# Kernel tuning notes

Hardware: AMD Instinct MI355X
Metric: run time of the kernel (lower is better)

Reference implementation:

```python
import jax, jax.numpy as jnp
import numpy as np
from jax import lax

BN_EPS = 1e-5
SP_NEAR = 2


def fps(xyz, m):
    # xyz: [b, n, c] -> indices [b, m]; deterministic start at index 0
    b, n, _ = xyz.shape
    def step(carry, _):
        dist, far = carry
        centroid = jnp.take_along_axis(xyz, far[:, None, None], axis=1)  # [b,1,c]
        d = jnp.sum((xyz - centroid) ** 2, axis=-1)                      # [b,n]
        dist = jnp.minimum(dist, d)
        return (dist, jnp.argmax(dist, axis=-1).astype(jnp.int32)), far
    init = (jnp.full((b, n), jnp.inf, xyz.dtype), jnp.zeros((b,), jnp.int32))
    _, idxs = lax.scan(step, init, None, length=m)
    return jnp.transpose(idxs)  # [b, m]


def knn(x, k):
    # x: [b, n, c] -> k nearest (incl. self) indices [b, n, k]
    sq = jnp.sum(x * x, axis=-1)
    d = sq[:, :, None] + sq[:, None, :] - 2.0 * jnp.einsum('bnc,bmc->bnm', x, x)
    return lax.top_k(-d, k)[1]


def gather_cf(x, idx):
    # channel-first index_points: x [b, c, n], idx [b, ...] -> [b, c, *idx.shape[1:]]
    b, c = x.shape[:2]
    flat = idx.reshape(b, -1)
    g = jnp.take_along_axis(x, flat[:, None, :], axis=2)
    return g.reshape((b, c) + idx.shape[1:])


def gather_cl(x, idx):
    # channel-last index_points: x [b, n, c], idx [b, ...] -> [b, *idx.shape[1:], c]
    b, c = x.shape[0], x.shape[-1]
    flat = idx.reshape(b, -1)
    g = jnp.take_along_axis(x, flat[:, :, None], axis=1)
    return g.reshape((b,) + idx.shape[1:] + (c,))


def bn_act(x, gamma, beta, nd):
    # inference-mode BatchNorm (running mean 0, var 1) + exact GELU; Dropout is identity in eval
    shp = (1, -1) + (1,) * nd
    scale = 1.0 / jnp.sqrt(1.0 + BN_EPS)
    return jax.nn.gelu(gamma.reshape(shp) * (x * scale) + beta.reshape(shp), approximate=False)


def setup_inputs() -> dict:
    key = jax.random.key(0)
    ks = jax.random.split(key, 8)
    BS, SP_IN, SP_OUT, DN_IN, DN_OUT = 128, 256, 256, 128, 128
    N_STK, N_STK_PNT, COOR = 32, 32, 32
    return {
        'sparse_fea': jax.random.normal(ks[0], (BS, SP_IN, N_STK), jnp.float32),
        'dense_fea': jax.random.normal(ks[1], (BS, DN_IN, N_STK, N_STK_PNT), jnp.float32),
        'stk_coor': jax.random.normal(ks[2], (BS, N_STK, COOR), jnp.float32),
        'n_stk_center': 16,
        'sp_w': jax.random.normal(ks[3], (SP_OUT, 2 * SP_IN), jnp.float32) * 0.02,
        'sp_b': jnp.zeros((SP_OUT,), jnp.float32),
        'sp_g': jnp.ones((SP_OUT,), jnp.float32),
        'sp_beta': jnp.zeros((SP_OUT,), jnp.float32),
        'dn_w': jax.random.normal(ks[4], (DN_OUT, 2 * DN_IN), jnp.float32) * 0.02,
        'dn_b': jnp.zeros((DN_OUT,), jnp.float32),
        'dn_g': jnp.ones((DN_OUT,), jnp.float32),
        'dn_beta': jnp.zeros((DN_OUT,), jnp.float32),
        'ds_w': jax.random.normal(ks[5], (DN_OUT, DN_IN, 1, 3), jnp.float32) * 0.05,
        'ds_b': jnp.zeros((DN_OUT,), jnp.float32),
        'ds_g': jnp.ones((DN_OUT,), jnp.float32),
        'ds_beta': jnp.zeros((DN_OUT,), jnp.float32),
    }


def reference(sparse_fea, dense_fea, stk_coor, n_stk_center,
              sp_w, sp_b, sp_g, sp_beta,
              dn_w, dn_b, dn_g, dn_beta,
              ds_w, ds_b, ds_g, ds_beta):
    bs, dn_in, n_stk, n_stk_pnt = dense_fea.shape
    fps_idx = fps(stk_coor, n_stk_center)            # [b, m]
    # --- sparse branch ---
    sc = gather_cf(sparse_fea, fps_idx)              # [b, c, m]
    knn_all = knn(stk_coor, SP_NEAR)                 # [b, n, k]
    knn_fps = gather_cl(knn_all, fps_idx)            # [b, m, k]
    sn = gather_cf(sparse_fea, knn_fps)              # [b, c, m, k]
    sa = sn - sc[:, :, :, None]
    sp_x = jnp.concatenate([sa, jnp.broadcast_to(sc[:, :, :, None], sa.shape)], axis=1)  # [b,2c,m,k]
    sp_x = jnp.einsum('bimk,oi->bomk', sp_x, sp_w) + sp_b[None, :, None, None]
    sp_x = bn_act(sp_x, sp_g, sp_beta, 2)
    sparse_out = jnp.max(sp_x, axis=3)               # [b, sp_out, m]
    # --- dense branch ---
    # 'b c s sp -> b s (sp c)'
    d_flat = jnp.transpose(dense_fea, (0, 2, 3, 1)).reshape(bs, n_stk, n_stk_pnt * dn_in)
    dc = gather_cl(d_flat, fps_idx)                  # [b, m, sp*c]
    dnb = gather_cl(d_flat, knn_fps)                 # [b, m, k, sp*c]
    da = dnb - dc[:, :, None, :]
    dcat = jnp.concatenate([da, jnp.broadcast_to(dc[:, :, None, :], da.shape)], axis=3)  # [b,m,k,2*sp*c]
    # 'b s n (sp c) -> b c s sp n' with sp=n_stk_pnt (exact torch reshape semantics)
    d5 = dcat.reshape(bs, fps_idx.shape[1], SP_NEAR, n_stk_pnt, 2 * dn_in)
    d5 = jnp.transpose(d5, (0, 4, 1, 3, 2))          # [b, 2c, m, sp, k]
    d5 = jnp.einsum('bimpn,oi->bompn', d5, dn_w) + dn_b[None, :, None, None, None]
    d5 = bn_act(d5, dn_g, dn_beta, 3)
    d4 = jnp.max(d5, axis=4)                         # [b, dn_out, m, sp]
    y = lax.conv_general_dilated(d4, ds_w, window_strides=(1, 2), padding=((0, 0), (1, 1)),
                                 dimension_numbers=('NCHW', 'OIHW', 'NCHW')) + ds_b[None, :, None, None]
    dense_out = bn_act(y, ds_g, ds_beta, 2)          # [b, dn_out, m, sp//2]
    coor_out = gather_cl(stk_coor, fps_idx)          # [b, m, coor]
    return sparse_out, dense_out, coor_out
```

## Files before the change

kernel.cpp:

```cpp
#include <hip/hip_runtime.h>


typedef unsigned short u16;
typedef unsigned int   u32;
typedef __attribute__((ext_vector_type(8))) short bf16x8;
typedef __attribute__((ext_vector_type(4))) float f32x4;

#define BN_SCALE 0.9999950000374997f

__device__ __forceinline__ float gelu_f(float x){
  return 0.5f*x*(1.0f + erff(x*0.70710678118654752f));
}
__device__ __forceinline__ u16 f2bf(float f){
  u32 x = __float_as_uint(f);
  x += 0x7fffu + ((x>>16)&1u);
  return (u16)(x>>16);
}

__global__ __launch_bounds__(256) void k_prep_fps(
    const float* __restrict__ dn_w, const float* __restrict__ ds_w, const float* __restrict__ sp_w,
    const float* __restrict__ coor,
    u16* __restrict__ wdb, u16* __restrict__ wcb, u16* __restrict__ wsb,
    int* __restrict__ fps_idx, int* __restrict__ nn_idx, float* __restrict__ coor_out)
{
  int blk = blockIdx.x, t = threadIdx.x;
  if (blk < 128){
    int w = blk*256 + t;
    int j=w&7, lane=(w>>3)&63, tile=w>>9;
    int kt=tile>>3, ot=tile&7;
    int o=ot*16+(lane&15), i=kt*32+(lane>>4)*8+j;
    wdb[w] = f2bf(dn_w[o*256+i]);
  } else if (blk < 320){
    int w = (blk-128)*256 + t;
    int j=w&7, lane=(w>>3)&63, tile=w>>9;
    int kt=tile>>3, ot=tile&7;
    int o=ot*16+(lane&15), k=kt*32+(lane>>4)*8+j;
    wcb[w] = f2bf(ds_w[o*384+k]);
  } else if (blk < 832){
    int w = (blk-320)*256 + t;
    int j=w&7, lane=(w>>3)&63, tile=w>>9;
    int kt=tile>>4, ot=tile&15;
    int o=ot*16+(lane&15), i=kt*32+(lane>>4)*8+j;
    wsb[w] = f2bf(sp_w[o*512+i]);
  } else {
    int b = blk - 832;
    __shared__ float Xs[32*33];
    __shared__ int s_sel[16];
    for (int i=t;i<1024;i+=256) Xs[(i>>5)*33 + (i&31)] = coor[b*1024+i];
    __syncthreads();
    if (t < 64){
      int j = t & 31;
      float xc[32];
      #pragma unroll
      for (int c=0;c<32;c++) xc[c] = Xs[j*33+c];
      float dist = 3.0e38f;
      int far = 0;
      int selv[16];
      #pragma unroll
      for (int it=0; it<16; ++it){
        selv[it] = far;
        const float* fc = &Xs[far*33];
        float d=0.f;
        #pragma unroll
        for (int c=0;c<32;c++){ float df=xc[c]-fc[c]; d+=df*df; }
        dist = fminf(dist,d);
        float v=dist; int idx=j;
        #pragma unroll
        for (int off=16; off>=1; off>>=1){
          float v2=__shfl_xor(v,off,32); int i2=__shfl_xor(idx,off,32);
          if (v2>v || (v2==v && i2<idx)){ v=v2; idx=i2; }
        }
        far = idx;
      }
      #pragma unroll
      for (int it=0; it<16; ++it){
        int sel = selv[it];
        const float* fc = &Xs[sel*33];
        float d=0.f;
        #pragma unroll
        for (int c=0;c<32;c++){ float df=xc[c]-fc[c]; d+=df*df; }
        if (j==sel) d=3.0e38f;
        float v=d; int idx=j;
        #pragma unroll
        for (int off=16; off>=1; off>>=1){
          float v2=__shfl_xor(v,off,32); int i2=__shfl_xor(idx,off,32);
          if (v2<v || (v2==v && i2<idx)){ v=v2; idx=i2; }
        }
        if (t==0){ nn_idx[b*16+it]=idx; fps_idx[b*16+it]=sel; s_sel[it]=sel; }
      }
    }
    __syncthreads();
    for (int q=t;q<512;q+=256){
      int mm=q>>5, c=q&31;
      coor_out[b*512+q] = Xs[s_sel[mm]*33 + c];
    }
  }
}

__global__ __launch_bounds__(256) void k_main(
    const float* __restrict__ sfea, const u16* __restrict__ wsb,
    const float* __restrict__ sp_b, const float* __restrict__ sp_g, const float* __restrict__ sp_be,
    const float* __restrict__ dfea, const u16* __restrict__ wdb,
    const float* __restrict__ dn_b, const float* __restrict__ dn_g, const float* __restrict__ dn_be,
    const u16* __restrict__ wcb,
    const float* __restrict__ ds_b, const float* __restrict__ ds_g, const float* __restrict__ ds_be,
    const int* __restrict__ fps_idx, const int* __restrict__ nn_idx,
    float* __restrict__ out_sp, float* __restrict__ out_dn)
{
  __shared__ char smem[20480];
  int blk=blockIdx.x;
  int t=threadIdx.x, lane=t&63, wv=t>>6, quad=lane>>4, col=lane&15;
  if (blk < 256){
    int b=blk>>1, oh=blk&1;
    u16*   Xb = (u16*)smem;
    float* P  = (float*)(smem+16640);
    int*   SI = (int*)(smem+19712);
    if (t<16){ SI[t]=fps_idx[b*16+t]&31; SI[16+t]=nn_idx[b*16+t]&31; }
    P[t]=sp_b[t]; P[256+t]=sp_g[t]; P[512+t]=sp_be[t];
    __syncthreads();
    const float* row = sfea + b*8192 + t*32;
    #pragma unroll
    for (int m=0;m<16;m++){
      float vc=row[SI[m]], vn=row[SI[16+m]];
      Xb[m*520 + t]       = f2bf(vn-vc);
      Xb[m*520 + 256 + t] = f2bf(vc);
    }
    __syncthreads();
    f32x4 accA[2]={}, accB[2]={};
    for (int kt=0;kt<8;kt++){
      bf16x8 bfr = *(const bf16x8*)&Xb[col*520 + kt*32 + quad*8];
      #pragma unroll
      for (int r=0;r<2;r++){
        int ot = oh*8 + wv + r*4;
        bf16x8 afr = *(const bf16x8*)&wsb[((kt*16+ot)*64+lane)*8];
        accA[r]=__builtin_amdgcn_mfma_f32_16x16x32_bf16(afr,bfr,accA[r],0,0,0);
      }
    }
    for (int kt=8;kt<16;kt++){
      bf16x8 bfr = *(const bf16x8*)&Xb[col*520 + kt*32 + quad*8];
      #pragma unroll
      for (int r=0;r<2;r++){
        int ot = oh*8 + wv + r*4;
        bf16x8 afr = *(const bf16x8*)&wsb[((kt*16+ot)*64+lane)*8];
        accB[r]=__builtin_amdgcn_mfma_f32_16x16x32_bf16(afr,bfr,accB[r],0,0,0);
      }
    }
    #pragma unroll
    for (int r=0;r<2;r++){
      #pragma unroll
      for (int reg=0;reg<4;reg++){
        int o = oh*128 + (wv+r*4)*16 + quad*4 + reg;
        float bo=P[o], go=P[256+o], be=P[512+o];
        float k1 = accA[r][reg]+accB[r][reg]+bo;
        float k0 = accB[r][reg]+bo;
        float v = fmaxf(gelu_f(go*(k1*BN_SCALE)+be), gelu_f(go*(k0*BN_SCALE)+be));
        out_sp[(b*256+o)*16 + col] = v;
      }
    }
  } else {
    int bd=blk-256; int b=bd>>4, m=bd&15;
    u16* Vb = (u16*)smem;
    u16* Bc = (u16*)smem;
    float* P = (float*)(smem+16896);
    int ci=fps_idx[bd]&31, ni=nn_idx[bd]&31;
    const float* Db = dfea + b*131072;
    if (t<128){
      P[t]=dn_b[t]; P[128+t]=dn_g[t]; P[256+t]=dn_be[t];
      P[384+t]=ds_b[t]; P[512+t]=ds_g[t]; P[640+t]=ds_be[t];
    }
    for (int fp=t; fp<2048; fp+=256){
      int c=fp>>4, xp=fp&15, x=xp*2;
      float2 fc = *(const float2*)(Db + c*1024 + ci*32 + x);
      float2 fn = *(const float2*)(Db + c*1024 + ni*32 + x);
      Vb[xp*264 + c]            = f2bf(fn.x-fc.x);
      Vb[(16+xp)*264 + c]       = f2bf(fc.x);
      Vb[xp*264 + 128 + c]      = f2bf(fn.y-fc.y);
      Vb[(16+xp)*264 + 128 + c] = f2bf(fc.y);
    }
    __syncthreads();
    if (t<128) P[768+t] = gelu_f(P[128+t]*(P[t]*BN_SCALE)+P[256+t]);
    f32x4 acc[2][2]={};
    for (int kt=0;kt<8;kt++){
      bf16x8 b0 = *(const bf16x8*)&Vb[ col     *264 + kt*32 + quad*8];
      bf16x8 b1 = *(const bf16x8*)&Vb[(16+col) *264 + kt*32 + quad*8];
      #pragma unroll
      for (int r=0;r<2;r++){
        int ot=wv+r*4;
        bf16x8 afr = *(const bf16x8*)&wdb[((kt*8+ot)*64+lane)*8];
        acc[r][0]=__builtin_amdgcn_mfma_f32_16x16x32_bf16(afr,b0,acc[r][0],0,0,0);
        acc[r][1]=__builtin_amdgcn_mfma_f32_16x16x32_bf16(afr,b1,acc[r][1],0,0,0);
      }
    }
    __syncthreads();
    for (int q=t; q<3136; q+=256) ((u32*)Bc)[q]=0u;
    __syncthreads();
    #pragma unroll
    for (int r=0;r<2;r++){
      #pragma unroll
      for (int pt=0;pt<2;pt++){
        #pragma unroll
        for (int reg=0;reg<4;reg++){
          int o = (wv+r*4)*16 + quad*4 + reg;
          int p = pt*16 + col;
          float bo=P[o], go=P[128+o], be=P[256+o];
          float val = gelu_f(go*((acc[r][pt][reg]+bo)*BN_SCALE)+be);
          if (pt==0) val = fmaxf(val, P[768+o]);
          u16 bv = f2bf(val);
          if (p&1){
            Bc[((p-1)>>1)*392 + o*3 + 2] = bv;
            if (p<31) Bc[((p+1)>>1)*392 + o*3 + 0] = bv;
          } else {
            Bc[(p>>1)*392 + o*3 + 1] = bv;
          }
        }
      }
    }
    __syncthreads();
    f32x4 cacc[2]={};
    for (int kt=0;kt<12;kt++){
      bf16x8 bfr = *(const bf16x8*)&Bc[col*392 + kt*32 + quad*8];
      #pragma unroll
      for (int r=0;r<2;r++){
        int ot=wv+r*4;
        bf16x8 afr = *(const bf16x8*)&wcb[((kt*8+ot)*64+lane)*8];
        cacc[r]=__builtin_amdgcn_mfma_f32_16x16x32_bf16(afr,bfr,cacc[r],0,0,0);
      }
    }
    #pragma unroll
    for (int r=0;r<2;r++){
      #pragma unroll
      for (int reg=0;reg<4;reg++){
        int o = (wv+r*4)*16 + quad*4 + reg;
        float cb=P[384+o], go=P[512+o], be=P[640+o];
        float val = gelu_f(go*((cacc[r][reg]+cb)*BN_SCALE)+be);
        out_dn[(b*128+o)*256 + m*16 + col] = val;
      }
    }
  }
}

extern "C" void kernel_launch(void* const* d_in, const int* in_sizes, int n_in,
                              void* d_out, int out_size, void* d_ws, size_t ws_size,
                              hipStream_t stream) {
  const float* sparse_fea = (const float*)d_in[0];
  const float* dense_fea  = (const float*)d_in[1];
  const float* stk_coor   = (const float*)d_in[2];
  const float* sp_w  = (const float*)d_in[4];
  const float* sp_b  = (const float*)d_in[5];
  const float* sp_g  = (const float*)d_in[6];
  const float* sp_be = (const float*)d_in[7];
  const float* dn_w  = (const float*)d_in[8];
  const float* dn_b  = (const float*)d_in[9];
  const float* dn_g  = (const float*)d_in[10];
  const float* dn_be = (const float*)d_in[11];
  const float* ds_w  = (const float*)d_in[12];
  const float* ds_b  = (const float*)d_in[13];
  const float* ds_g  = (const float*)d_in[14];
  const float* ds_be = (const float*)d_in[15];

  float* out = (float*)d_out;
  int* fps_idx = (int*)d_ws;
  int* nn_idx  = fps_idx + 2048;
  u16* wdb = (u16*)((char*)d_ws + 16384);
  u16* wcb = (u16*)((char*)d_ws + 81920);
  u16* wsb = (u16*)((char*)d_ws + 180224);

  k_prep_fps<<<960, 256, 0, stream>>>(dn_w, ds_w, sp_w, stk_coor,
                                      wdb, wcb, wsb, fps_idx, nn_idx, out + 4718592);
  k_main    <<<2304, 256, 0, stream>>>(sparse_fea, wsb, sp_b, sp_g, sp_be,
                                       dense_fea, wdb, dn_b, dn_g, dn_be,
                                       wcb, ds_b, ds_g, ds_be,
                                       fps_idx, nn_idx, out, out + 524288);
}
```

Measured before the change: 179.5 us.

## Split FPS into own kernel with precomputed distance matrix, remap blocks, shrink LDS

Moves farthest-point sampling and kNN out of the weight-conversion kernel into a separate launch. It precomputes the full 32x32 pairwise distance matrix in shared memory using all 256 threads, then runs the serial FPS loop on table lookups and spreads the nearest-neighbour search across four waves. The main kernel remaps block indices so groups of 8 batches are interleaved, and reuses shared memory so the parameter buffers overlap the staging buffers, cutting LDS per block. The cost is an extra kernel launch and additional barriers in the main kernel.

```diff
diff --git a/kernel.cpp b/kernel.cpp
--- a/kernel.cpp
+++ b/kernel.cpp
@@ -17,83 +17,92 @@
   return (u16)(x>>16);
 }
 
-__global__ __launch_bounds__(256) void k_prep_fps(
+__global__ __launch_bounds__(256) void k_weights(
     const float* __restrict__ dn_w, const float* __restrict__ ds_w, const float* __restrict__ sp_w,
-    const float* __restrict__ coor,
-    u16* __restrict__ wdb, u16* __restrict__ wcb, u16* __restrict__ wsb,
-    int* __restrict__ fps_idx, int* __restrict__ nn_idx, float* __restrict__ coor_out)
+    u16* __restrict__ wdb, u16* __restrict__ wcb, u16* __restrict__ wsb)
 {
   int blk = blockIdx.x, t = threadIdx.x;
   if (blk < 128){
     int w = blk*256 + t;
     int j=w&7, lane=(w>>3)&63, tile=w>>9;
     int kt=tile>>3, ot=tile&7;
-    int o=ot*16+(lane&15), i=kt*32+(lane>>4)*8+j;
+    int o=ot*16+(lane&15), i=kt*32+((lane>>4)&3)*8+j;
     wdb[w] = f2bf(dn_w[o*256+i]);
   } else if (blk < 320){
     int w = (blk-128)*256 + t;
     int j=w&7, lane=(w>>3)&63, tile=w>>9;
     int kt=tile>>3, ot=tile&7;
-    int o=ot*16+(lane&15), k=kt*32+(lane>>4)*8+j;
+    int o=ot*16+(lane&15), k=kt*32+((lane>>4)&3)*8+j;
     wcb[w] = f2bf(ds_w[o*384+k]);
-  } else if (blk < 832){
+  } else {
     int w = (blk-320)*256 + t;
     int j=w&7, lane=(w>>3)&63, tile=w>>9;
     int kt=tile>>4, ot=tile&15;
-    int o=ot*16+(lane&15), i=kt*32+(lane>>4)*8+j;
+    int o=ot*16+(lane&15), i=kt*32+((lane>>4)&3)*8+j;
     wsb[w] = f2bf(sp_w[o*512+i]);
-  } else {
-    int b = blk - 832;
-    __shared__ float Xs[32*33];
-    __shared__ int s_sel[16];
-    for (int i=t;i<1024;i+=256) Xs[(i>>5)*33 + (i&31)] = coor[b*1024+i];
-    __syncthreads();
-    if (t < 64){
-      int j = t & 31;
-      float xc[32];
-      #pragma unroll
-      for (int c=0;c<32;c++) xc[c] = Xs[j*33+c];
-      float dist = 3.0e38f;
-      int far = 0;
-      int selv[16];
-      #pragma unroll
-      for (int it=0; it<16; ++it){
-        selv[it] = far;
-        const float* fc = &Xs[far*33];
-        float d=0.f;
-        #pragma unroll
-        for (int c=0;c<32;c++){ float df=xc[c]-fc[c]; d+=df*df; }
-        dist = fminf(dist,d);
-        float v=dist; int idx=j;
-        #pragma unroll
-        for (int off=16; off>=1; off>>=1){
-          float v2=__shfl_xor(v,off,32); int i2=__shfl_xor(idx,off,32);
-          if (v2>v || (v2==v && i2<idx)){ v=v2; idx=i2; }
-        }
-        far = idx;
-      }
-      #pragma unroll
-      for (int it=0; it<16; ++it){
-        int sel = selv[it];
-        const float* fc = &Xs[sel*33];
-        float d=0.f;
-        #pragma unroll
-        for (int c=0;c<32;c++){ float df=xc[c]-fc[c]; d+=df*df; }
-        if (j==sel) d=3.0e38f;
-        float v=d; int idx=j;
-        #pragma unroll
-        for (int off=16; off>=1; off>>=1){
-          float v2=__shfl_xor(v,off,32); int i2=__shfl_xor(idx,off,32);
-          if (v2<v || (v2==v && i2<idx)){ v=v2; idx=i2; }
-        }
-        if (t==0){ nn_idx[b*16+it]=idx; fps_idx[b*16+it]=sel; s_sel[it]=sel; }
-      }
-    }
-    __syncthreads();
-    for (int q=t;q<512;q+=256){
-      int mm=q>>5, c=q&31;
-      coor_out[b*512+q] = Xs[s_sel[mm]*33 + c];
-    }
+  }
+}
+
+__global__ __launch_bounds__(256) void k_fps(
+    const float* __restrict__ coor,
+    int* __restrict__ fps_idx, int* __restrict__ nn_idx, float* __restrict__ coor_out)
+{
+  int b = blockIdx.x, t = threadIdx.x;
+  __shared__ float Xs[32*33];
+  __shared__ float D[32*33];
+  __shared__ int   s_sel[16];
+  for (int i=t;i<1024;i+=256) Xs[(i>>5)*33 + (i&31)] = coor[b*1024+i];
+  __syncthreads();
+  #pragma unroll
+  for (int k2=0;k2<4;k2++){
+    int p=t+k2*256, i=p>>5, j=p&31;
+    float d=0.f;
+    #pragma unroll
+    for (int c=0;c<32;c++){ float df=Xs[i*33+c]-Xs[j*33+c]; d+=df*df; }
+    D[i*33+j]=d;
+  }
+  __syncthreads();
+  if (t < 64){
+    int j = t & 31;
+    float dist = 3.0e38f;
+    int far = 0;
+    #pragma unroll
+    for (int it=0; it<16; ++it){
+      if (t==0) s_sel[it]=far;
+      dist = fminf(dist, D[far*33+j]);
+      float v=dist; int idx=j;
+      #pragma unroll
+      for (int off=16; off>=1; off>>=1){
+        float v2=__shfl_xor(v,off,32); int i2=__shfl_xor(idx,off,32);
+        if (v2>v || (v2==v && i2<idx)){ v=v2; idx=i2; }
+      }
+      far = idx;
+    }
+    if (t==0){
+      #pragma unroll
+      for (int it=0;it<16;++it) fps_idx[b*16+it]=s_sel[it];
+    }
+  }
+  __syncthreads();
+  {
+    int wv=t>>6, j=t&31;
+    #pragma unroll
+    for (int q=0;q<4;q++){
+      int it = wv*4+q, sel = s_sel[it];
+      float d = D[sel*33+j];
+      if (j==sel) d=3.0e38f;
+      float v=d; int idx=j;
+      #pragma unroll
+      for (int off=16; off>=1; off>>=1){
+        float v2=__shfl_xor(v,off,32); int i2=__shfl_xor(idx,off,32);
+        if (v2<v || (v2==v && i2<idx)){ v=v2; idx=i2; }
+      }
+      if ((t&63)==0) nn_idx[b*16+it]=idx;
+    }
+  }
+  for (int q=t;q<512;q+=256){
+    int mm=q>>5, c=q&31;
+    coor_out[b*512+q] = Xs[s_sel[mm]*33 + c];
   }
 }
 
@@ -107,16 +116,15 @@
     const int* __restrict__ fps_idx, const int* __restrict__ nn_idx,
     float* __restrict__ out_sp, float* __restrict__ out_dn)
 {
-  __shared__ char smem[20480];
+  __shared__ char smem[16896];
   int blk=blockIdx.x;
   int t=threadIdx.x, lane=t&63, wv=t>>6, quad=lane>>4, col=lane&15;
   if (blk < 256){
-    int b=blk>>1, oh=blk&1;
+    int b = ((blk>>4)<<3) | (blk&7), oh = (blk>>3)&1;
     u16*   Xb = (u16*)smem;
-    float* P  = (float*)(smem+16640);
-    int*   SI = (int*)(smem+19712);
+    float* P  = (float*)smem;
+    __shared__ int SI[32];
     if (t<16){ SI[t]=fps_idx[b*16+t]&31; SI[16+t]=nn_idx[b*16+t]&31; }
-    P[t]=sp_b[t]; P[256+t]=sp_g[t]; P[512+t]=sp_be[t];
     __syncthreads();
     const float* row = sfea + b*8192 + t*32;
     #pragma unroll
@@ -145,6 +153,9 @@
         accB[r]=__builtin_amdgcn_mfma_f32_16x16x32_bf16(afr,bfr,accB[r],0,0,0);
       }
     }
+    __syncthreads();
+    P[t]=sp_b[t]; P[256+t]=sp_g[t]; P[512+t]=sp_be[t];
+    __syncthreads();
     #pragma unroll
     for (int r=0;r<2;r++){
       #pragma unroll
@@ -158,16 +169,14 @@
       }
     }
   } else {
-    int bd=blk-256; int b=bd>>4, m=bd&15;
+    int d=blk-256;
+    int b = ((d>>7)<<3) | (d&7), m = (d>>3)&15;
     u16* Vb = (u16*)smem;
     u16* Bc = (u16*)smem;
-    float* P = (float*)(smem+16896);
-    int ci=fps_idx[bd]&31, ni=nn_idx[bd]&31;
+    float* P = (float*)(smem+12544);
+    int mi = b*16+m;
+    int ci=fps_idx[mi]&31, ni=nn_idx[mi]&31;
     const float* Db = dfea + b*131072;
-    if (t<128){
-      P[t]=dn_b[t]; P[128+t]=dn_g[t]; P[256+t]=dn_be[t];
-      P[384+t]=ds_b[t]; P[512+t]=ds_g[t]; P[640+t]=ds_be[t];
-    }
     for (int fp=t; fp<2048; fp+=256){
       int c=fp>>4, xp=fp&15, x=xp*2;
       float2 fc = *(const float2*)(Db + c*1024 + ci*32 + x);
@@ -178,7 +187,6 @@
       Vb[(16+xp)*264 + 128 + c] = f2bf(fc.y);
     }
     __syncthreads();
-    if (t<128) P[768+t] = gelu_f(P[128+t]*(P[t]*BN_SCALE)+P[256+t]);
     f32x4 acc[2][2]={};
     for (int kt=0;kt<8;kt++){
       bf16x8 b0 = *(const bf16x8*)&Vb[ col     *264 + kt*32 + quad*8];
@@ -193,6 +201,12 @@
     }
     __syncthreads();
     for (int q=t; q<3136; q+=256) ((u32*)Bc)[q]=0u;
+    if (t<128){
+      float b0=dn_b[t], g0=dn_g[t], e0=dn_be[t];
+      P[t]=b0; P[128+t]=g0; P[256+t]=e0;
+      P[384+t]=ds_b[t]; P[512+t]=ds_g[t]; P[640+t]=ds_be[t];
+      P[768+t]=gelu_f(g0*(b0*BN_SCALE)+e0);
+    }
     __syncthreads();
     #pragma unroll
     for (int r=0;r<2;r++){
@@ -265,10 +279,10 @@
   u16* wcb = (u16*)((char*)d_ws + 81920);
   u16* wsb = (u16*)((char*)d_ws + 180224);
 
-  k_prep_fps<<<960, 256, 0, stream>>>(dn_w, ds_w, sp_w, stk_coor,
-                                      wdb, wcb, wsb, fps_idx, nn_idx, out + 4718592);
-  k_main    <<<2304, 256, 0, stream>>>(sparse_fea, wsb, sp_b, sp_g, sp_be,
-                                       dense_fea, wdb, dn_b, dn_g, dn_be,
-                                       wcb, ds_b, ds_g, ds_be,
-                                       fps_idx, nn_idx, out, out + 524288);
-}
+  k_fps    <<<128, 256, 0, stream>>>(stk_coor, fps_idx, nn_idx, out + 4718592);
+  k_weights<<<832, 256, 0, stream>>>(dn_w, ds_w, sp_w, wdb, wcb, wsb);
+  k_main   <<<2304, 256, 0, stream>>>(sparse_fea, wsb, sp_b, sp_g, sp_be,
+                                      dense_fea, wdb, dn_b, dn_g, dn_be,
+                                      wcb, ds_b, ds_g, ds_be,
+                                      fps_idx, nn_idx, out, out + 524288);
+}
```

Result: faster. 172.1 us (-4.1%).
